# Kernel optimization log

Measured on AMD Instinct MI355X. Metric: run time of the kernel, lower is better.

## Reference

```python
import jax, jax.numpy as jnp
from jax import lax
import numpy as np

B, C, H, W = 32, 256, 56, 56
K = 3
EPS = 1e-5


def setup_inputs() -> dict:
    key = jax.random.key(0)
    k1, k2, k3, k4 = jax.random.split(key, 4)
    x = jax.random.normal(k1, (B, C, H, W), dtype=jnp.float32)
    # xavier_normal init for conv weight [C_out, C_in, K, K]
    fan_in = C * K * K
    fan_out = C * K * K
    std = float(np.sqrt(2.0 / (fan_in + fan_out)))
    w = jax.random.normal(k2, (C, C, K, K), dtype=jnp.float32) * std
    gamma = jnp.ones((C,), dtype=jnp.float32)
    beta = jnp.zeros((C,), dtype=jnp.float32)
    return {"x": x, "w": w, "gamma": gamma, "beta": beta}


def reference(x, w, gamma, beta):
    # --- Binarize (bi_act_method=0, bi_w_scale=1) ---
    bx = jnp.sign(x)                                   # activation sign
    wc = jnp.clip(w, -1.0, 1.0)                        # fp_weight.data.clamp_(-1,1)
    mean_val = jnp.mean(jnp.abs(wc))
    bw = jnp.sign(wc) * mean_val                       # sign(w) * mean(|w|)
    # --- float conv2d, stride 1, padding 1 ---
    out = lax.conv_general_dilated(
        bx, bw, window_strides=(1, 1), padding=[(1, 1), (1, 1)],
        dimension_numbers=("NCHW", "OIHW", "NCHW"))
    # --- identity shortcut (stride=1, C_in==C_out) ---
    out = out + x
    # --- BatchNorm2d (training-mode batch stats, affine) ---
    mean = jnp.mean(out, axis=(0, 2, 3), keepdims=True)
    var = jnp.var(out, axis=(0, 2, 3), keepdims=True)
    out = (out - mean) * lax.rsqrt(var + EPS)
    out = out * gamma[None, :, None, None] + beta[None, :, None, None]
    # --- ReLU ---
    return jax.nn.relu(out)
```

## Files before the change

kernel.cpp:

```cpp
#include <hip/hip_runtime.h>
#include <cstdint>

#define Bn   32
#define Cn   256
#define Hn   56
#define Wn   56
#define HWn  (Hn*Wn)
#define NPIX (Bn*HWn)
#define WELEMS (Cn*Cn*9)
#define EPSv 1e-5f

#define PR   58
#define PPLANE (PR*PR)

#define F_WABS  0
#define F_SUM   64
#define F_SQ    320
#define STATS_BYTES 4096
#define WPK_OFF  4096
#define WPK_BYTES WELEMS
#define ACT_OFF  (WPK_OFF + WPK_BYTES)
#define ACT_BYTES (Bn*PPLANE*Cn)

typedef int v4i __attribute__((ext_vector_type(4)));

__global__ void pack_all(const float* __restrict__ x,
                         const float* __restrict__ w,
                         float* __restrict__ wsf,
                         uint8_t* __restrict__ wpk,
                         uint8_t* __restrict__ act) {
    if (blockIdx.x < 392) {
        int v = blockIdx.x * 256 + threadIdx.x;
        if (v < 7296) {
            int b = v / 228;
            int r = v - b * 228;
            int y, xx;
            if (r < 58)       { y = 0;  xx = r; }
            else if (r < 116) { y = 57; xx = r - 58; }
            else { int r2 = r - 116; y = 1 + (r2 >> 1); xx = (r2 & 1) * 57; }
            uint4* d = (uint4*)(act + ((size_t)(b * PR + y) * PR + xx) * 256);
            uint4 z = make_uint4(0, 0, 0, 0);
            #pragma unroll
            for (int i = 0; i < 16; i++) d[i] = z;
        }
        int b = v / HWn;
        int p = v - b * HWn;
        int y = p / Wn;
        int xx = p - y * Wn;
        const float* xp = x + (size_t)b * Cn * HWn + p;
        int key = (xx + 1) & 15;
        uint32_t* dst = (uint32_t*)(act + ((size_t)(b * PR + (y + 1)) * PR + (xx + 1)) * 256);
        #pragma unroll
        for (int slot = 0; slot < 16; slot++) {
            uint32_t rr[4];
            #pragma unroll
            for (int cw = 0; cw < 4; cw++) {
                uint32_t r = 0;
                #pragma unroll
                for (int j = 0; j < 4; j++) {
                    uint32_t sgn = __float_as_uint(xp[(size_t)(slot * 16 + cw * 4 + j) * HWn]) >> 31;
                    r |= (sgn ? 0xFFu : 0x01u) << (j * 8);
                }
                rr[cw] = r;
            }
            *(uint4*)(dst + (size_t)((slot ^ key) * 4)) = make_uint4(rr[0], rr[1], rr[2], rr[3]);
        }
    } else {
        int u = (blockIdx.x - 392) * 256 + threadIdx.x;
        int co = u / 36;
        int kc = u - co * 36;
        int t  = kc >> 2;
        int s  = kc & 3;
        const float* wp = w + (size_t)co * 2304 + t;
        uint32_t* dst = (uint32_t*)(wpk + ((size_t)kc * 256 + co) * 64);
        float sabs = 0.0f;
        #pragma unroll
        for (int cw = 0; cw < 16; cw++) {
            uint32_t r = 0;
            #pragma unroll
            for (int j = 0; j < 4; j++) {
                int ci = s * 64 + cw * 4 + j;
                float wv = wp[(size_t)ci * 9];
                sabs += fminf(fabsf(wv), 1.0f);
                r |= ((__float_as_uint(wv) >> 31) ? 0xFFu : 0x01u) << (j * 8);
            }
            dst[cw] = r;
        }
        #pragma unroll
        for (int off = 32; off; off >>= 1) sabs += __shfl_down(sabs, off);
        __shared__ float sh[4];
        if ((threadIdx.x & 63) == 0) sh[threadIdx.x >> 6] = sabs;
        __syncthreads();
        if (threadIdx.x == 0)
            atomicAdd(&wsf[F_WABS], sh[0] + sh[1] + sh[2] + sh[3]);
    }
}

__global__ __launch_bounds__(256, 2) void conv_mfma(
    const uint8_t* __restrict__ act, const uint8_t* __restrict__ wpk,
    const float* __restrict__ x, float* __restrict__ wsf,
    float* __restrict__ out) {
    __shared__ uint4 ldsv[3712];
    uint8_t* lds = (uint8_t*)ldsv;

    const int tid  = threadIdx.x;
    const int lane = tid & 63;
    const int wid  = tid >> 6;
    const int l15  = lane & 15;
    const int l4   = lane >> 4;

    const int bx = blockIdx.x;
    const int b  = bx / 28;
    const int y0 = (bx - b * 28) * 2;

    {
        const uint4* src = (const uint4*)(act + ((size_t)b * PR + y0) * PR * 256);
        for (int i = tid; i < 3712; i += 256) ldsv[i] = src[i];
    }

    const uint8_t* abase = wpk + (wid * 64 + l15) * 64 + l4 * 16;

    v4i af0[4], af1[4];
    #pragma unroll
    for (int mi = 0; mi < 4; mi++) {
        af0[mi] = *(const v4i*)(abase + (size_t)0 * 16384 + mi * 1024);
        af1[mi] = *(const v4i*)(abase + (size_t)1 * 16384 + mi * 1024);
    }

    int pixb[7], key[7];
    #pragma unroll
    for (int ni = 0; ni < 7; ni++) {
        int n  = ni * 16 + l15;
        int r_ = n / 56;
        int c_ = n - r_ * 56;
        pixb[ni] = (r_ * 58 + c_) * 256;
        key[ni]  = c_ & 15;
    }

    __syncthreads();

    v4i bfA[7], bfB[7];
    #pragma unroll
    for (int ni = 0; ni < 7; ni++)
        bfA[ni] = *(const v4i*)(lds + pixb[ni] + ((l4 ^ key[ni]) << 4));

    v4i acc[4][7] = {};

#define STEP(SP, BFC, BFN, AF, KCN)                                            \
    {                                                                          \
        _Pragma("unroll")                                                      \
        for (int ni = 0; ni < 7; ni++)                                         \
            BFN[ni] = *(const v4i*)(lds + pixb[ni] +                           \
                                    ((((SP) * 4 + l4) ^ key[ni]) << 4));       \
        _Pragma("unroll")                                                      \
        for (int ni = 0; ni < 7; ni++) {                                       \
            _Pragma("unroll")                                                  \
            for (int mi = 0; mi < 4; mi++)                                     \
                acc[mi][ni] = __builtin_amdgcn_mfma_i32_16x16x64_i8(           \
                    AF[mi], BFC[ni], acc[mi][ni], 0, 0, 0);                    \
        }                                                                      \
        {                                                                      \
            int kcn = (KCN) > 35 ? 35 : (KCN);                                 \
            const uint8_t* ap = abase + (size_t)kcn * 16384;                   \
            _Pragma("unroll")                                                  \
            for (int mi = 0; mi < 4; mi++)                                     \
                AF[mi] = *(const v4i*)(ap + mi * 1024);                        \
        }                                                                      \
    }

    #pragma unroll 1
    for (int t = 0; t < 9; t++) {
        const int t4 = t * 4;
        const int wrap  = (t == 2 || t == 5);
        const int dtoff = (t == 8) ? 0 : (wrap ? 56 * 256 : 256);
        const int ddw   = (t == 8) ? 0 : (wrap ? -2 : 1);

        STEP(1, bfA, bfB, af0, t4 + 2)
        STEP(2, bfB, bfA, af1, t4 + 3)
        STEP(3, bfA, bfB, af0, t4 + 4)
        #pragma unroll
        for (int ni = 0; ni < 7; ni++) {
            pixb[ni] += dtoff;
            key[ni]   = (key[ni] + ddw) & 15;
        }
        STEP(0, bfB, bfA, af1, t4 + 5)
    }
#undef STEP

    const float mv = wsf[F_WABS] * (1.0f / (float)WELEMS);
    const int co_w = wid * 64;
    const int pbase = b * (Cn * HWn) + y0 * 56;

    float ssum[4][4] = {}, ssq[4][4] = {};
    #pragma unroll
    for (int mi = 0; mi < 4; mi++) {
        #pragma unroll
        for (int ni = 0; ni < 7; ni++) {
            v4i a = acc[mi][ni];
            #pragma unroll
            for (int q = 0; q < 4; q++) {
                int co = co_w + mi * 16 + l4 * 4 + q;
                size_t idx = (size_t)pbase + (size_t)co * HWn + (ni * 16 + l15);
                float val = fmaf(mv, (float)a[q], x[idx]);
                out[idx] = val;
                ssum[mi][q] += val;
                ssq[mi][q]  += val * val;
            }
        }
    }
    #pragma unroll
    for (int mi = 0; mi < 4; mi++) {
        #pragma unroll
        for (int q = 0; q < 4; q++) {
            float s = ssum[mi][q], sq = ssq[mi][q];
            #pragma unroll
            for (int off = 1; off < 16; off <<= 1) {
                s  += __shfl_xor(s, off);
                sq += __shfl_xor(sq, off);
            }
            if (l15 == 0) {
                int co = co_w + mi * 16 + l4 * 4 + q;
                atomicAdd(&wsf[F_SUM + co], s);
                atomicAdd(&wsf[F_SQ  + co], sq);
            }
        }
    }
}

__global__ void epilogue_kernel(float* __restrict__ out,
                                const float* __restrict__ wsf,
                                const float* __restrict__ g,
                                const float* __restrict__ bt) {
    int plane = blockIdx.x;
    int c = plane & 255;
    const float n = (float)(Bn * HWn);
    float mean = wsf[F_SUM + c] / n;
    float var  = wsf[F_SQ + c] / n - mean * mean;
    float sc = g[c] * rsqrtf(var + EPSv);
    float sh = bt[c] - mean * sc;
    float4* o4 = (float4*)(out + (size_t)plane * HWn);
    for (int i = threadIdx.x; i < HWn / 4; i += 256) {
        float4 v = o4[i];
        v.x = fmaxf(fmaf(v.x, sc, sh), 0.0f);
        v.y = fmaxf(fmaf(v.y, sc, sh), 0.0f);
        v.z = fmaxf(fmaf(v.z, sc, sh), 0.0f);
        v.w = fmaxf(fmaf(v.w, sc, sh), 0.0f);
        o4[i] = v;
    }
}

extern "C" void kernel_launch(void* const* d_in, const int* in_sizes, int n_in,
                              void* d_out, int out_size, void* d_ws, size_t ws_size,
                              hipStream_t stream) {
    const float* x     = (const float*)d_in[0];
    const float* w     = (const float*)d_in[1];
    const float* gamma = (const float*)d_in[2];
    const float* beta  = (const float*)d_in[3];
    float* out = (float*)d_out;

    float*   wsf = (float*)d_ws;
    uint8_t* wpk = (uint8_t*)d_ws + WPK_OFF;
    uint8_t* act = (uint8_t*)d_ws + ACT_OFF;

    hipMemsetAsync(d_ws, 0, STATS_BYTES, stream);
    pack_all<<<dim3(428), dim3(256), 0, stream>>>(x, w, wsf, wpk, act);
    conv_mfma<<<dim3(896), dim3(256), 0, stream>>>(act, wpk, x, wsf, out);
    epilogue_kernel<<<dim3(Bn * Cn), dim3(256), 0, stream>>>(out, wsf, gamma, beta);
}
```

Before: 357.6 us.

## Split conv output channels across eight waves with smaller per-wave tiles

```diff
diff --git a/kernel.cpp b/kernel.cpp
--- a/kernel.cpp
+++ b/kernel.cpp
@@ -96,7 +96,7 @@
     }
 }
 
-__global__ __launch_bounds__(256, 2) void conv_mfma(
+__global__ __launch_bounds__(512, 4) void conv_mfma(
     const uint8_t* __restrict__ act, const uint8_t* __restrict__ wpk,
     const float* __restrict__ x, float* __restrict__ wsf,
     float* __restrict__ out) {
@@ -115,17 +115,15 @@
 
     {
         const uint4* src = (const uint4*)(act + ((size_t)b * PR + y0) * PR * 256);
-        for (int i = tid; i < 3712; i += 256) ldsv[i] = src[i];
-    }
-
-    const uint8_t* abase = wpk + (wid * 64 + l15) * 64 + l4 * 16;
-
-    v4i af0[4], af1[4];
-    #pragma unroll
-    for (int mi = 0; mi < 4; mi++) {
-        af0[mi] = *(const v4i*)(abase + (size_t)0 * 16384 + mi * 1024);
-        af1[mi] = *(const v4i*)(abase + (size_t)1 * 16384 + mi * 1024);
-    }
+        for (int i = tid; i < 3712; i += 512) ldsv[i] = src[i];
+    }
+
+    const uint8_t* abase = wpk + (wid * 32 + l15) * 64 + l4 * 16;
+
+    v4i af[2];
+    #pragma unroll
+    for (int mi = 0; mi < 2; mi++)
+        af[mi] = *(const v4i*)(abase + mi * 1024);
 
     int pixb[7], key[7];
     #pragma unroll
@@ -139,61 +137,56 @@
 
     __syncthreads();
 
-    v4i bfA[7], bfB[7];
-    #pragma unroll
-    for (int ni = 0; ni < 7; ni++)
-        bfA[ni] = *(const v4i*)(lds + pixb[ni] + ((l4 ^ key[ni]) << 4));
-
-    v4i acc[4][7] = {};
-
-#define STEP(SP, BFC, BFN, AF, KCN)                                            \
+    v4i acc[2][7] = {};
+
+#define STEP(S, KCN)                                                           \
     {                                                                          \
+        v4i bf[7];                                                             \
         _Pragma("unroll")                                                      \
         for (int ni = 0; ni < 7; ni++)                                         \
-            BFN[ni] = *(const v4i*)(lds + pixb[ni] +                           \
-                                    ((((SP) * 4 + l4) ^ key[ni]) << 4));       \
+            bf[ni] = *(const v4i*)(lds + pixb[ni] +                            \
+                                   ((((S) * 4 + l4) ^ key[ni]) << 4));         \
         _Pragma("unroll")                                                      \
         for (int ni = 0; ni < 7; ni++) {                                       \
             _Pragma("unroll")                                                  \
-            for (int mi = 0; mi < 4; mi++)                                     \
+            for (int mi = 0; mi < 2; mi++)                                     \
                 acc[mi][ni] = __builtin_amdgcn_mfma_i32_16x16x64_i8(           \
-                    AF[mi], BFC[ni], acc[mi][ni], 0, 0, 0);                    \
+                    af[mi], bf[ni], acc[mi][ni], 0, 0, 0);                     \
         }                                                                      \
         {                                                                      \
             int kcn = (KCN) > 35 ? 35 : (KCN);                                 \
             const uint8_t* ap = abase + (size_t)kcn * 16384;                   \
             _Pragma("unroll")                                                  \
-            for (int mi = 0; mi < 4; mi++)                                     \
-                AF[mi] = *(const v4i*)(ap + mi * 1024);                        \
+            for (int mi = 0; mi < 2; mi++)                                     \
+                af[mi] = *(const v4i*)(ap + mi * 1024);                        \
         }                                                                      \
     }
 
     #pragma unroll 1
     for (int t = 0; t < 9; t++) {
         const int t4 = t * 4;
+        STEP(0, t4 + 1)
+        STEP(1, t4 + 2)
+        STEP(2, t4 + 3)
+        STEP(3, t4 + 4)
         const int wrap  = (t == 2 || t == 5);
         const int dtoff = (t == 8) ? 0 : (wrap ? 56 * 256 : 256);
         const int ddw   = (t == 8) ? 0 : (wrap ? -2 : 1);
-
-        STEP(1, bfA, bfB, af0, t4 + 2)
-        STEP(2, bfB, bfA, af1, t4 + 3)
-        STEP(3, bfA, bfB, af0, t4 + 4)
         #pragma unroll
         for (int ni = 0; ni < 7; ni++) {
             pixb[ni] += dtoff;
             key[ni]   = (key[ni] + ddw) & 15;
         }
-        STEP(0, bfB, bfA, af1, t4 + 5)
     }
 #undef STEP
 
     const float mv = wsf[F_WABS] * (1.0f / (float)WELEMS);
-    const int co_w = wid * 64;
+    const int co_w = wid * 32;
     const int pbase = b * (Cn * HWn) + y0 * 56;
 
-    float ssum[4][4] = {}, ssq[4][4] = {};
-    #pragma unroll
-    for (int mi = 0; mi < 4; mi++) {
+    float ssum[2][4] = {}, ssq[2][4] = {};
+    #pragma unroll
+    for (int mi = 0; mi < 2; mi++) {
         #pragma unroll
         for (int ni = 0; ni < 7; ni++) {
             v4i a = acc[mi][ni];
@@ -209,7 +202,7 @@
         }
     }
     #pragma unroll
-    for (int mi = 0; mi < 4; mi++) {
+    for (int mi = 0; mi < 2; mi++) {
         #pragma unroll
         for (int q = 0; q < 4; q++) {
             float s = ssum[mi][q], sq = ssq[mi][q];
@@ -264,6 +257,6 @@
 
     hipMemsetAsync(d_ws, 0, STATS_BYTES, stream);
     pack_all<<<dim3(428), dim3(256), 0, stream>>>(x, w, wsf, wpk, act);
-    conv_mfma<<<dim3(896), dim3(256), 0, stream>>>(act, wpk, x, wsf, out);
+    conv_mfma<<<dim3(896), dim3(512), 0, stream>>>(act, wpk, x, wsf, out);
     epilogue_kernel<<<dim3(Bn * Cn), dim3(256), 0, stream>>>(out, wsf, gamma, beta);
 }
```

New measurement: 372.8 us. +4.3%, slower.
